# Optimization experiments

Hardware: AMD Instinct MI355X
Metric: run time of the kernel (lower is better)

The kernel has to match this reference:

```python
import jax, jax.numpy as jnp
import numpy as np

EMBED_DIM = 1024
NUM_HEADS = 16
HEAD_DIM = EMBED_DIM // NUM_HEADS
B, S = 2, 2048


def _xavier(k, shape):
    # xavier_uniform for square [out,in] weight
    limit = float(np.sqrt(6.0 / (shape[0] + shape[1])))
    return jax.random.uniform(k, shape, jnp.float32, -limit, limit)


def setup_inputs() -> dict:
    key = jax.random.key(0)
    ks = jax.random.split(key, 7)
    return {
        "query": jax.random.normal(ks[0], (B, S, EMBED_DIM), jnp.float32),
        "key": jax.random.normal(ks[1], (B, S, EMBED_DIM), jnp.float32),
        "value": jax.random.normal(ks[2], (B, S, EMBED_DIM), jnp.float32),
        "Wq": _xavier(ks[3], (EMBED_DIM, EMBED_DIM)),
        "Wk": _xavier(ks[4], (EMBED_DIM, EMBED_DIM)),
        "Wv": _xavier(ks[5], (EMBED_DIM, EMBED_DIM)),
        "Wo": _xavier(ks[6], (EMBED_DIM, EMBED_DIM)),
    }


def _orthogonalize(Wq, Wk):
    # Both projections computed from the ORIGINAL weights, then both replaced
    # (matches torch: weight1_proj/weight2_proj computed before copy_).
    Wq_o = Wq - Wq @ (Wk.T @ Wk)
    Wk_o = Wk - Wk @ (Wq.T @ Wq)
    return Wq_o, Wk_o


def reference(query, key, value, Wq, Wk, Wv, Wo):
    Wq_o, Wk_o = _orthogonalize(Wq, Wk)
    # F.linear(x, W) = x @ W.T
    q = query @ Wq_o.T
    k = key @ Wk_o.T
    v = value @ Wv.T
    # [B, S, E] -> [B, H, S, Dh]
    def split_heads(x):
        return x.reshape(B, -1, NUM_HEADS, HEAD_DIM).transpose(0, 2, 1, 3)
    q, k, v = split_heads(q), split_heads(k), split_heads(v)
    scale = 1.0 / (HEAD_DIM ** 0.5)
    scores = jnp.einsum("bhqd,bhkd->bhqk", q, k) * scale
    attn = jax.nn.softmax(scores, axis=-1)
    out = jnp.einsum("bhqk,bhkd->bhqd", attn, v)
    out = out.transpose(0, 2, 1, 3).reshape(B, -1, EMBED_DIM)
    return out @ Wo.T
```

## Files before the change

kernel.cpp:

```cpp
#include <hip/hip_runtime.h>
#include <math.h>

constexpr int EMBED  = 1024;
constexpr int NHEADS = 16;
constexpr int HDIM   = 64;
constexpr int BATCH  = 2;
constexpr int SEQ    = 2048;
constexpr int MROWS  = BATCH * SEQ;

typedef unsigned short u16b;
typedef __attribute__((ext_vector_type(8))) short bfrag;
typedef __attribute__((ext_vector_type(4))) float ffrag;
typedef __attribute__((ext_vector_type(16))) float f16frag;
typedef __attribute__((ext_vector_type(4))) int i32x4;

#define SCALE_Q 0.18033688f

__device__ __forceinline__ u16b f2b(float f) {
    union { float f; unsigned u; } v; v.f = f;
    unsigned r = v.u + 0x7fffu + ((v.u >> 16) & 1u);
    return (u16b)(r >> 16);
}

__device__ __forceinline__ unsigned cvtpk_bf16(float a, float b) {
    unsigned r;
    asm("v_cvt_pk_bf16_f32 %0, %1, %2" : "=v"(r) : "v"(a), "v"(b));
    return r;
}

__device__ __forceinline__ void plane_swap(unsigned a, unsigned b, int& lo, int& hi) {
    auto r = __builtin_amdgcn_permlane32_swap((int)a, (int)b, false, false);
    lo = (int)r[0];
    hi = (int)r[1];
}

__device__ __forceinline__ void gload_lds16(const u16b* g, u16b* l) {
    __builtin_amdgcn_global_load_lds(
        (const __attribute__((address_space(1))) void*)g,
        (__attribute__((address_space(3))) void*)l,
        16, 0, 0);
}

template<int N>
__device__ __forceinline__ void wait_vmcnt() {
    if constexpr (N == 0)      asm volatile("s_waitcnt vmcnt(0)" ::: "memory");
    else if constexpr (N == 3) asm volatile("s_waitcnt vmcnt(3)" ::: "memory");
    else if constexpr (N == 4) asm volatile("s_waitcnt vmcnt(4)" ::: "memory");
    else static_assert(N == 0 || N == 3 || N == 4, "unsupported vmcnt");
}

struct GemmPtrs {
    const u16b* A[3];
    const u16b* B[3];
    const float* D[3];
    u16b* Cb[3];
    float* Cf[3];
    float scale[3];
    int vt[3];
    int hs[3];
};

__global__ void prep_all(const float* __restrict__ q, const float* __restrict__ k,
                         const float* __restrict__ v,
                         const float* __restrict__ Wq, const float* __restrict__ Wk,
                         const float* __restrict__ Wv, const float* __restrict__ Wo,
                         u16b* __restrict__ oq, u16b* __restrict__ ok, u16b* __restrict__ ov,
                         u16b* __restrict__ wq, u16b* __restrict__ wk,
                         u16b* __restrict__ wv, u16b* __restrict__ wo,
                         u16b* __restrict__ wqt, u16b* __restrict__ wkt) {
    const int z = blockIdx.z;
    const int tid = threadIdx.x;
    if (z < 3) {
        const float* src = (z == 0) ? q : (z == 1) ? k : v;
        u16b* dst = (z == 0) ? oq : (z == 1) ? ok : ov;
        const int i = blockIdx.x * 256 + tid;
        float4 val = ((const float4*)src)[i];
        ushort4 o;
        o.x = f2b(val.x); o.y = f2b(val.y); o.z = f2b(val.z); o.w = f2b(val.w);
        ((ushort4*)dst)[i] = o;
        return;
    }
    if (blockIdx.x >= 1024) return;
    const int w = z - 3;
    const float* src = (w == 0) ? Wq : (w == 1) ? Wk : (w == 2) ? Wv : Wo;
    u16b* dst  = (w == 0) ? wq : (w == 1) ? wk : (w == 2) ? wv : wo;
    u16b* dstT = (w == 0) ? wqt : (w == 1) ? wkt : nullptr;
    __shared__ float t[32][33];
    const int bx = (blockIdx.x & 31) * 32, by = (blockIdx.x >> 5) * 32;
    const int x = tid & 31, y = tid >> 5;
#pragma unroll
    for (int r = 0; r < 4; ++r) {
        const int row = by + y + 8 * r;
        const float val = src[(size_t)row * EMBED + bx + x];
        dst[(size_t)row * EMBED + bx + x] = f2b(val);
        if (w < 2) t[y + 8 * r][x] = val;
    }
    if (w >= 2) return;
    __syncthreads();
#pragma unroll
    for (int r = 0; r < 4; ++r)
        dstT[(size_t)(bx + y + 8 * r) * EMBED + by + x] = f2b(t[x][y + 8 * r]);
}

template<int MODE, int BM>
__global__ __launch_bounds__(256) void gemm_big(GemmPtrs p, int M, int N, int K) {
    const int z = blockIdx.z;
    const u16b* __restrict__ A = p.A[z];
    const u16b* __restrict__ B = p.B[z];
    const float* __restrict__ D = p.D[z];
    u16b* __restrict__ Cb = p.Cb[z];
    float* __restrict__ Cf = p.Cf[z];
    const float scale = p.scale[z];
    const int vt = p.vt[z], hs = p.hs[z];

    constexpr int BK = 32;
    constexpr int IT = BM / 32;
    constexpr int IA = BM / 64;
    constexpr int LPW = IA + 2;
    __shared__ __align__(16) u16b As[2][BM * BK];
    __shared__ __align__(16) u16b Bs[2][128 * BK];

    const int tid = threadIdx.x;
    const int wave = tid >> 6, lane = tid & 63;
    const int quad = lane >> 4, l16 = lane & 15;
    const int wrow = wave >> 1, wcol = wave & 1;
    const int m0 = blockIdx.y * BM, n0 = blockIdx.x * 128;

    ffrag acc[IT][4];
#pragma unroll
    for (int i = 0; i < IT; ++i)
#pragma unroll
        for (int j = 0; j < 4; ++j) acc[i][j] = ffrag{0.f, 0.f, 0.f, 0.f};

    const int srow = lane >> 2, schunk = lane & 3;

    auto STAGE = [&](int buf, int kt) {
#pragma unroll
        for (int q = 0; q < IA; ++q) {
            int row = wave * (BM / 4) + q * 16;
            gload_lds16(A + (size_t)(m0 + row + srow) * K + kt + schunk * 8,
                        &As[buf][row * BK]);
        }
#pragma unroll
        for (int q = 0; q < 2; ++q) {
            int row = wave * 32 + q * 16;
            gload_lds16(B + (size_t)(n0 + row + srow) * K + kt + schunk * 8,
                        &Bs[buf][row * BK]);
        }
    };

    STAGE(0, 0);
    STAGE(1, BK);
    wait_vmcnt<LPW>();
    __builtin_amdgcn_s_barrier();
    __builtin_amdgcn_sched_barrier(0);

    int cur = 0;
    for (int kt = 0; kt < K; kt += BK, cur ^= 1) {
        bfrag af[IT], bfv[4];
#pragma unroll
        for (int i = 0; i < IT; ++i)
            af[i] = *(const bfrag*)&As[cur][(wrow * (BM / 2) + i * 16 + l16) * BK + quad * 8];
#pragma unroll
        for (int j = 0; j < 4; ++j)
            bfv[j] = *(const bfrag*)&Bs[cur][(wcol * 64 + j * 16 + l16) * BK + quad * 8];
        asm volatile("s_waitcnt lgkmcnt(0)" ::: "memory");
        __builtin_amdgcn_sched_barrier(0);
        __builtin_amdgcn_s_barrier();
        __builtin_amdgcn_sched_barrier(0);

        const bool stage = (kt + 2 * BK < K);
        if (stage) STAGE(cur, kt + 2 * BK);

#pragma unroll
        for (int i = 0; i < IT; ++i)
#pragma unroll
            for (int j = 0; j < 4; ++j)
                acc[i][j] = __builtin_amdgcn_mfma_f32_16x16x32_bf16(af[i], bfv[j], acc[i][j], 0, 0, 0);

        if (stage) wait_vmcnt<LPW>();
        else       wait_vmcnt<0>();
        __builtin_amdgcn_s_barrier();
        __builtin_amdgcn_sched_barrier(0);
    }

    if (MODE == 0 && vt) {
#pragma unroll
        for (int i = 0; i < IT; ++i)
#pragma unroll
            for (int j = 0; j < 4; ++j) {
                const int col = n0 + wcol * 64 + j * 16 + l16;
                const int h = col >> 6, d = col & 63;
                const int row0 = m0 + wrow * (BM / 2) + i * 16 + quad * 4;
                const int b = row0 >> 11, s = row0 & 2047;
                ushort4 o;
                o.x = f2b(acc[i][j][0]); o.y = f2b(acc[i][j][1]);
                o.z = f2b(acc[i][j][2]); o.w = f2b(acc[i][j][3]);
                *(ushort4*)&Cb[((size_t)(b * NHEADS + h) * HDIM + d) * SEQ + s] = o;
            }
        return;
    }
    if (MODE == 0 && hs) {
#pragma unroll
        for (int i = 0; i < IT; ++i)
#pragma unroll
            for (int j = 0; j < 4; ++j) {
                const int col = n0 + wcol * 64 + j * 16 + l16;
                const int h = col >> 6, d = col & 63;
                const int row0 = m0 + wrow * (BM / 2) + i * 16 + quad * 4;
                const int b = row0 >> 11, s0 = row0 & 2047;
#pragma unroll
                for (int r = 0; r < 4; ++r)
                    Cb[((size_t)(b * NHEADS + h) * SEQ + s0 + r) * HDIM + d] =
                        f2b(acc[i][j][r] * scale);
            }
        return;
    }

#pragma unroll
    for (int i = 0; i < IT; ++i)
#pragma unroll
        for (int j = 0; j < 4; ++j) {
            const int col = n0 + wcol * 64 + j * 16 + l16;
#pragma unroll
            for (int r = 0; r < 4; ++r) {
                const int row = m0 + wrow * (BM / 2) + i * 16 + quad * 4 + r;
                const size_t idx = (size_t)row * N + col;
                const float v = acc[i][j][r];
                if (MODE == 0) Cb[idx] = f2b(v * scale);
                else if (MODE == 1) Cb[idx] = f2b(D[idx] - v);
                else Cf[idx] = v;
            }
        }
}

__global__ __launch_bounds__(256) void flash_attn6(
    const u16b* __restrict__ Qp, const u16b* __restrict__ Kp,
    const u16b* __restrict__ Vt, float* __restrict__ Opart,
    float* __restrict__ Lpart)
{
    const int tid = threadIdx.x;
    const int wave = tid >> 6, lane = tid & 63;
    const int l32 = lane & 31, hi = lane >> 5;
    const int qt = blockIdx.x, h = blockIdx.y;
    const int b = blockIdx.z >> 1, sp = blockIdx.z & 1;
    const int qb = qt * 128 + wave * 32;
    const int kt0 = sp * (SEQ / 2), kt1 = kt0 + SEQ / 2;

    __shared__ __align__(16) u16b Ks[2][64 * 64];
    __shared__ __align__(16) u16b Vs[2][64 * 64];

    const size_t hsbase = (size_t)(b * NHEADS + h) * SEQ;
    const size_t vtbase = (size_t)(b * NHEADS + h) * HDIM * SEQ;
    const size_t obase  = ((size_t)sp * MROWS + (size_t)b * SEQ) * EMBED + h * HDIM;

    bfrag bq[4];
#pragma unroll
    for (int ks = 0; ks < 4; ++ks)
        bq[ks] = *(const bfrag*)&Qp[(hsbase + qb + l32) * HDIM + ks * 16 + hi * 8];

    f16frag ov0, ov1;
#pragma unroll
    for (int r = 0; r < 16; ++r) { ov0[r] = 0.f; ov1[r] = 0.f; }
    float l_run = 0.f;

    const int r0 = tid >> 3, c0 = tid & 7;
    const int sw0 = (r0 * 8 + (c0 ^ (r0 & 7))) * 8;
    const int sw1 = ((r0 + 32) * 8 + (c0 ^ (r0 & 7))) * 8;
    const u16b* kgb = Kp + hsbase * HDIM;
    const u16b* vgb = Vt + vtbase;

    {
        const u16b* kg = kgb + (size_t)kt0 * HDIM;
        bfrag k0 = *(const bfrag*)(kg + tid * 8);
        bfrag k1 = *(const bfrag*)(kg + (tid + 256) * 8);
        bfrag v0 = *(const bfrag*)(vgb + (size_t)r0 * SEQ + kt0 + c0 * 8);
        bfrag v1 = *(const bfrag*)(vgb + (size_t)(r0 + 32) * SEQ + kt0 + c0 * 8);
        *(bfrag*)&Ks[0][sw0] = k0;  *(bfrag*)&Ks[0][sw1] = k1;
        *(bfrag*)&Vs[0][sw0] = v0;  *(bfrag*)&Vs[0][sw1] = v1;
    }
    __syncthreads();

    int p = 0;
    for (int kt = kt0; kt < kt1; kt += 64, p ^= 1) {
        const bool more = (kt + 64) < kt1;
        bfrag kn0, kn1, vn0, vn1;
        if (more) {
            const u16b* kg = kgb + (size_t)(kt + 64) * HDIM;
            kn0 = *(const bfrag*)(kg + tid * 8);
            kn1 = *(const bfrag*)(kg + (tid + 256) * 8);
            vn0 = *(const bfrag*)(vgb + (size_t)r0 * SEQ + kt + 64 + c0 * 8);
            vn1 = *(const bfrag*)(vgb + (size_t)(r0 + 32) * SEQ + kt + 64 + c0 * 8);
        }

        f16frag St0, St1;
#pragma unroll
        for (int r = 0; r < 16; ++r) { St0[r] = 0.f; St1[r] = 0.f; }
#pragma unroll
        for (int ks = 0; ks < 4; ++ks) {
            const int ch = ks * 2 + hi;
            bfrag k0 = *(const bfrag*)&Ks[p][(l32 * 8 + (ch ^ (l32 & 7))) * 8];
            bfrag k1 = *(const bfrag*)&Ks[p][((32 + l32) * 8 + (ch ^ (l32 & 7))) * 8];
            St0 = __builtin_amdgcn_mfma_f32_32x32x16_bf16(k0, bq[ks], St0, 0, 0, 0);
            St1 = __builtin_amdgcn_mfma_f32_32x32x16_bf16(k1, bq[ks], St1, 0, 0, 0);
        }

        float rs = 0.f;
#pragma unroll
        for (int r = 0; r < 16; ++r) {
            const float a = __builtin_amdgcn_exp2f(St0[r]);
            const float c = __builtin_amdgcn_exp2f(St1[r]);
            St0[r] = a; St1[r] = c;
            rs += a + c;
        }
        rs += __shfl_xor(rs, 32);
        l_run += rs;

        unsigned d0[8], d1[8];
#pragma unroll
        for (int rr = 0; rr < 8; ++rr) {
            d0[rr] = cvtpk_bf16(St0[2 * rr], St0[2 * rr + 1]);
            d1[rr] = cvtpk_bf16(St1[2 * rr], St1[2 * rr + 1]);
        }
        bfrag bp[4];
        {
            int a0, a1, b0, b1, c0w, c1, e0, e1;
            plane_swap(d0[0], d0[2], a0, a1);
            plane_swap(d0[1], d0[3], b0, b1);
            i32x4 w = { a0, b0, a1, b1 };
            bp[0] = __builtin_bit_cast(bfrag, w);
            plane_swap(d0[4], d0[6], c0w, c1);
            plane_swap(d0[5], d0[7], e0, e1);
            i32x4 w2 = { c0w, e0, c1, e1 };
            bp[1] = __builtin_bit_cast(bfrag, w2);
        }
        {
            int a0, a1, b0, b1, c0w, c1, e0, e1;
            plane_swap(d1[0], d1[2], a0, a1);
            plane_swap(d1[1], d1[3], b0, b1);
            i32x4 w = { a0, b0, a1, b1 };
            bp[2] = __builtin_bit_cast(bfrag, w);
            plane_swap(d1[4], d1[6], c0w, c1);
            plane_swap(d1[5], d1[7], e0, e1);
            i32x4 w2 = { c0w, e0, c1, e1 };
            bp[3] = __builtin_bit_cast(bfrag, w2);
        }

#pragma unroll
        for (int ks = 0; ks < 4; ++ks) {
            const int ch = ks * 2 + hi;
            bfrag v0 = *(const bfrag*)&Vs[p][(l32 * 8 + (ch ^ (l32 & 7))) * 8];
            bfrag v1 = *(const bfrag*)&Vs[p][((32 + l32) * 8 + (ch ^ (l32 & 7))) * 8];
            ov0 = __builtin_amdgcn_mfma_f32_32x32x16_bf16(v0, bp[ks], ov0, 0, 0, 0);
            ov1 = __builtin_amdgcn_mfma_f32_32x32x16_bf16(v1, bp[ks], ov1, 0, 0, 0);
        }

        if (more) {
            *(bfrag*)&Ks[p ^ 1][sw0] = kn0;  *(bfrag*)&Ks[p ^ 1][sw1] = kn1;
            *(bfrag*)&Vs[p ^ 1][sw0] = vn0;  *(bfrag*)&Vs[p ^ 1][sw1] = vn1;
            __syncthreads();
        }
    }

    const size_t orow = obase + (size_t)(qb + l32) * EMBED;
#pragma unroll
    for (int rr = 0; rr < 4; ++rr) {
        float4 o0, o1;
        o0.x = ov0[4 * rr + 0]; o0.y = ov0[4 * rr + 1];
        o0.z = ov0[4 * rr + 2]; o0.w = ov0[4 * rr + 3];
        o1.x = ov1[4 * rr + 0]; o1.y = ov1[4 * rr + 1];
        o1.z = ov1[4 * rr + 2]; o1.w = ov1[4 * rr + 3];
        *(float4*)&Opart[orow + rr * 8 + hi * 4] = o0;
        *(float4*)&Opart[orow + 32 + rr * 8 + hi * 4] = o1;
    }
    if (hi == 0)
        Lpart[((size_t)sp * BATCH * NHEADS + b * NHEADS + h) * SEQ + qb + l32] = l_run;
}

__global__ void combine_o(const float* __restrict__ O0, const float* __restrict__ O1,
                          const float* __restrict__ L0, const float* __restrict__ L1,
                          u16b* __restrict__ ao) {
    const int i = blockIdx.x * 256 + threadIdx.x;
    const int e0 = i << 2;
    const int row = e0 >> 10, col = e0 & 1023;
    const int lidx = ((row >> 11) * NHEADS + (col >> 6)) * SEQ + (row & 2047);
    float4 a = ((const float4*)O0)[i];
    float4 c = ((const float4*)O1)[i];
    const float inv = 1.f / (L0[lidx] + L1[lidx]);
    ushort4 o;
    o.x = f2b((a.x + c.x) * inv); o.y = f2b((a.y + c.y) * inv);
    o.z = f2b((a.z + c.z) * inv); o.w = f2b((a.w + c.w) * inv);
    ((ushort4*)ao)[i] = o;
}

extern "C" void kernel_launch(void* const* d_in, const int* in_sizes, int n_in,
                              void* d_out, int out_size, void* d_ws, size_t ws_size,
                              hipStream_t stream) {
    const float* query = (const float*)d_in[0];
    const float* key_  = (const float*)d_in[1];
    const float* value = (const float*)d_in[2];
    const float* Wq    = (const float*)d_in[3];
    const float* Wk    = (const float*)d_in[4];
    const float* Wv    = (const float*)d_in[5];
    const float* Wo    = (const float*)d_in[6];
    float* out = (float*)d_out;

    char* ws = (char*)d_ws;
    const size_t MB = 1024 * 1024;
    u16b* xq  = (u16b*)(ws + 0 * MB);
    u16b* xk  = (u16b*)(ws + 8 * MB);
    u16b* xv  = (u16b*)(ws + 16 * MB);
    u16b* wq  = (u16b*)(ws + 24 * MB);
    u16b* wk  = (u16b*)(ws + 26 * MB);
    u16b* wv  = (u16b*)(ws + 28 * MB);
    u16b* gq  = (u16b*)(ws + 32 * MB);
    u16b* gk  = (u16b*)(ws + 34 * MB);
    u16b* wqo = (u16b*)(ws + 36 * MB);
    u16b* wko = (u16b*)(ws + 38 * MB);
    u16b* wo  = (u16b*)(ws + 40 * MB);
    u16b* qp  = (u16b*)(ws + 44 * MB);
    u16b* kp  = (u16b*)(ws + 52 * MB);
    u16b* Vt  = (u16b*)(ws + 60 * MB);
    u16b* wqt = (u16b*)(ws + 60 * MB);
    u16b* wkt = (u16b*)(ws + 62 * MB);
    float* Op  = (float*)(ws + 0 * MB);
    float* Lp  = (float*)(ws + 32 * MB);
    u16b*  ao  = (u16b*)(ws + 44 * MB);

    prep_all<<<dim3(MROWS * EMBED / 1024, 1, 7), dim3(256), 0, stream>>>(
        query, key_, value, Wq, Wk, Wv, Wo,
        xq, xk, xv, wq, wk, wv, wo, wqt, wkt);

    {
        GemmPtrs p{};
        p.A[0] = wqt; p.B[0] = wqt; p.Cb[0] = gq; p.scale[0] = 1.f;
        p.A[1] = wkt; p.B[1] = wkt; p.Cb[1] = gk; p.scale[1] = 1.f;
        gemm_big<0, 64><<<dim3(EMBED / 128, EMBED / 64, 2), dim3(256), 0, stream>>>(
            p, EMBED, EMBED, EMBED);
    }
    {
        GemmPtrs p{};
        p.A[0] = wq; p.B[0] = gk; p.D[0] = Wq; p.Cb[0] = wqo;
        p.A[1] = wk; p.B[1] = gq; p.D[1] = Wk; p.Cb[1] = wko;
        gemm_big<1, 64><<<dim3(EMBED / 128, EMBED / 64, 2), dim3(256), 0, stream>>>(
            p, EMBED, EMBED, EMBED);
    }
    {
        GemmPtrs p{};
        p.A[0] = xq; p.B[0] = wqo; p.Cb[0] = qp; p.scale[0] = SCALE_Q; p.hs[0] = 1;
        p.A[1] = xk; p.B[1] = wko; p.Cb[1] = kp; p.scale[1] = 1.f;     p.hs[1] = 1;
        p.A[2] = xv; p.B[2] = wv;  p.Cb[2] = Vt; p.scale[2] = 1.f;     p.vt[2] = 1;
        gemm_big<0, 128><<<dim3(EMBED / 128, MROWS / 128, 3), dim3(256), 0, stream>>>(
            p, MROWS, EMBED, EMBED);
    }
    flash_attn6<<<dim3(SEQ / 128, NHEADS, BATCH * 2), dim3(256), 0, stream>>>(
        qp, kp, Vt, Op, Lp);
    combine_o<<<dim3(MROWS * EMBED / 1024), dim3(256), 0, stream>>>(
        Op, Op + (size_t)MROWS * EMBED, Lp, Lp + (size_t)BATCH * NHEADS * SEQ, ao);
    {
        GemmPtrs p{};
        p.A[0] = ao; p.B[0] = wo; p.Cf[0] = out; p.scale[0] = 1.f;
        gemm_big<2, 64><<<dim3(EMBED / 128, MROWS / 64, 1), dim3(256), 0, stream>>>(
            p, MROWS, EMBED, EMBED);
    }
}
```

Baseline: 276.9 us.

## Load attention K/V fragments directly from global memory and add GEMM BN template

The flash attention kernel no longer stages K and V tiles through double-buffered shared memory with barriers. Each wave now loads its K and V MFMA fragments straight from global memory in 32-key steps and prefetches the next K fragments into registers. This removes LDS traffic and __syncthreads, but every wave now fetches K/V redundantly from global/L2 and gets less work per step. Separately, the GEMM gains a BN template parameter so the small weight-weight GEMMs use 64x64 tiles, giving more blocks.

```diff
diff --git a/kernel.cpp b/kernel.cpp
--- a/kernel.cpp
+++ b/kernel.cpp
@@ -44,9 +44,10 @@
 template<int N>
 __device__ __forceinline__ void wait_vmcnt() {
     if constexpr (N == 0)      asm volatile("s_waitcnt vmcnt(0)" ::: "memory");
+    else if constexpr (N == 2) asm volatile("s_waitcnt vmcnt(2)" ::: "memory");
     else if constexpr (N == 3) asm volatile("s_waitcnt vmcnt(3)" ::: "memory");
     else if constexpr (N == 4) asm volatile("s_waitcnt vmcnt(4)" ::: "memory");
-    else static_assert(N == 0 || N == 3 || N == 4, "unsupported vmcnt");
+    else static_assert(N == 0 || N == 2 || N == 3 || N == 4, "unsupported vmcnt");
 }
 
 struct GemmPtrs {
@@ -102,7 +103,7 @@
         dstT[(size_t)(bx + y + 8 * r) * EMBED + by + x] = f2b(t[x][y + 8 * r]);
 }
 
-template<int MODE, int BM>
+template<int MODE, int BM, int BN>
 __global__ __launch_bounds__(256) void gemm_big(GemmPtrs p, int M, int N, int K) {
     const int z = blockIdx.z;
     const u16b* __restrict__ A = p.A[z];
@@ -115,22 +116,24 @@
 
     constexpr int BK = 32;
     constexpr int IT = BM / 32;
+    constexpr int JT = BN / 32;
     constexpr int IA = BM / 64;
-    constexpr int LPW = IA + 2;
+    constexpr int IB = BN / 64;
+    constexpr int LPW = IA + IB;
     __shared__ __align__(16) u16b As[2][BM * BK];
-    __shared__ __align__(16) u16b Bs[2][128 * BK];
+    __shared__ __align__(16) u16b Bs[2][BN * BK];
 
     const int tid = threadIdx.x;
     const int wave = tid >> 6, lane = tid & 63;
     const int quad = lane >> 4, l16 = lane & 15;
     const int wrow = wave >> 1, wcol = wave & 1;
-    const int m0 = blockIdx.y * BM, n0 = blockIdx.x * 128;
-
-    ffrag acc[IT][4];
+    const int m0 = blockIdx.y * BM, n0 = blockIdx.x * BN;
+
+    ffrag acc[IT][JT];
 #pragma unroll
     for (int i = 0; i < IT; ++i)
 #pragma unroll
-        for (int j = 0; j < 4; ++j) acc[i][j] = ffrag{0.f, 0.f, 0.f, 0.f};
+        for (int j = 0; j < JT; ++j) acc[i][j] = ffrag{0.f, 0.f, 0.f, 0.f};
 
     const int srow = lane >> 2, schunk = lane & 3;
 
@@ -142,8 +145,8 @@
                         &As[buf][row * BK]);
         }
 #pragma unroll
-        for (int q = 0; q < 2; ++q) {
-            int row = wave * 32 + q * 16;
+        for (int q = 0; q < IB; ++q) {
+            int row = wave * (BN / 4) + q * 16;
             gload_lds16(B + (size_t)(n0 + row + srow) * K + kt + schunk * 8,
                         &Bs[buf][row * BK]);
         }
@@ -157,13 +160,13 @@
 
     int cur = 0;
     for (int kt = 0; kt < K; kt += BK, cur ^= 1) {
-        bfrag af[IT], bfv[4];
+        bfrag af[IT], bfv[JT];
 #pragma unroll
         for (int i = 0; i < IT; ++i)
             af[i] = *(const bfrag*)&As[cur][(wrow * (BM / 2) + i * 16 + l16) * BK + quad * 8];
 #pragma unroll
-        for (int j = 0; j < 4; ++j)
-            bfv[j] = *(const bfrag*)&Bs[cur][(wcol * 64 + j * 16 + l16) * BK + quad * 8];
+        for (int j = 0; j < JT; ++j)
+            bfv[j] = *(const bfrag*)&Bs[cur][(wcol * (BN / 2) + j * 16 + l16) * BK + quad * 8];
         asm volatile("s_waitcnt lgkmcnt(0)" ::: "memory");
         __builtin_amdgcn_sched_barrier(0);
         __builtin_amdgcn_s_barrier();
@@ -175,7 +178,7 @@
 #pragma unroll
         for (int i = 0; i < IT; ++i)
 #pragma unroll
-            for (int j = 0; j < 4; ++j)
+            for (int j = 0; j < JT; ++j)
                 acc[i][j] = __builtin_amdgcn_mfma_f32_16x16x32_bf16(af[i], bfv[j], acc[i][j], 0, 0, 0);
 
         if (stage) wait_vmcnt<LPW>();
@@ -188,8 +191,8 @@
 #pragma unroll
         for (int i = 0; i < IT; ++i)
 #pragma unroll
-            for (int j = 0; j < 4; ++j) {
-                const int col = n0 + wcol * 64 + j * 16 + l16;
+            for (int j = 0; j < JT; ++j) {
+                const int col = n0 + wcol * (BN / 2) + j * 16 + l16;
                 const int h = col >> 6, d = col & 63;
                 const int row0 = m0 + wrow * (BM / 2) + i * 16 + quad * 4;
                 const int b = row0 >> 11, s = row0 & 2047;
@@ -204,8 +207,8 @@
 #pragma unroll
         for (int i = 0; i < IT; ++i)
 #pragma unroll
-            for (int j = 0; j < 4; ++j) {
-                const int col = n0 + wcol * 64 + j * 16 + l16;
+            for (int j = 0; j < JT; ++j) {
+                const int col = n0 + wcol * (BN / 2) + j * 16 + l16;
                 const int h = col >> 6, d = col & 63;
                 const int row0 = m0 + wrow * (BM / 2) + i * 16 + quad * 4;
                 const int b = row0 >> 11, s0 = row0 & 2047;
@@ -220,8 +223,8 @@
 #pragma unroll
     for (int i = 0; i < IT; ++i)
 #pragma unroll
-        for (int j = 0; j < 4; ++j) {
-            const int col = n0 + wcol * 64 + j * 16 + l16;
+        for (int j = 0; j < JT; ++j) {
+            const int col = n0 + wcol * (BN / 2) + j * 16 + l16;
 #pragma unroll
             for (int r = 0; r < 4; ++r) {
                 const int row = m0 + wrow * (BM / 2) + i * 16 + quad * 4 + r;
@@ -234,7 +237,7 @@
         }
 }
 
-__global__ __launch_bounds__(256) void flash_attn6(
+__global__ __launch_bounds__(256) void flash_attn7(
     const u16b* __restrict__ Qp, const u16b* __restrict__ Kp,
     const u16b* __restrict__ Vt, float* __restrict__ Opart,
     float* __restrict__ Lpart)
@@ -247,9 +250,6 @@
     const int qb = qt * 128 + wave * 32;
     const int kt0 = sp * (SEQ / 2), kt1 = kt0 + SEQ / 2;
 
-    __shared__ __align__(16) u16b Ks[2][64 * 64];
-    __shared__ __align__(16) u16b Vs[2][64 * 64];
-
     const size_t hsbase = (size_t)(b * NHEADS + h) * SEQ;
     const size_t vtbase = (size_t)(b * NHEADS + h) * HDIM * SEQ;
     const size_t obase  = ((size_t)sp * MROWS + (size_t)b * SEQ) * EMBED + h * HDIM;
@@ -264,101 +264,71 @@
     for (int r = 0; r < 16; ++r) { ov0[r] = 0.f; ov1[r] = 0.f; }
     float l_run = 0.f;
 
-    const int r0 = tid >> 3, c0 = tid & 7;
-    const int sw0 = (r0 * 8 + (c0 ^ (r0 & 7))) * 8;
-    const int sw1 = ((r0 + 32) * 8 + (c0 ^ (r0 & 7))) * 8;
     const u16b* kgb = Kp + hsbase * HDIM;
     const u16b* vgb = Vt + vtbase;
 
-    {
-        const u16b* kg = kgb + (size_t)kt0 * HDIM;
-        bfrag k0 = *(const bfrag*)(kg + tid * 8);
-        bfrag k1 = *(const bfrag*)(kg + (tid + 256) * 8);
-        bfrag v0 = *(const bfrag*)(vgb + (size_t)r0 * SEQ + kt0 + c0 * 8);
-        bfrag v1 = *(const bfrag*)(vgb + (size_t)(r0 + 32) * SEQ + kt0 + c0 * 8);
-        *(bfrag*)&Ks[0][sw0] = k0;  *(bfrag*)&Ks[0][sw1] = k1;
-        *(bfrag*)&Vs[0][sw0] = v0;  *(bfrag*)&Vs[0][sw1] = v1;
-    }
-    __syncthreads();
-
-    int p = 0;
-    for (int kt = kt0; kt < kt1; kt += 64, p ^= 1) {
-        const bool more = (kt + 64) < kt1;
-        bfrag kn0, kn1, vn0, vn1;
+    bfrag kf[4];
+#pragma unroll
+    for (int ks = 0; ks < 4; ++ks)
+        kf[ks] = *(const bfrag*)&kgb[(size_t)(kt0 + l32) * HDIM + ks * 16 + hi * 8];
+
+    for (int kt = kt0; kt < kt1; kt += 32) {
+        f16frag St;
+#pragma unroll
+        for (int r = 0; r < 16; ++r) St[r] = 0.f;
+#pragma unroll
+        for (int ks = 0; ks < 4; ++ks)
+            St = __builtin_amdgcn_mfma_f32_32x32x16_bf16(kf[ks], bq[ks], St, 0, 0, 0);
+
+        bfrag vf0[2], vf1[2], kn[4];
+        const bool more = (kt + 32) < kt1;
+#pragma unroll
+        for (int s = 0; s < 2; ++s) {
+            vf0[s] = *(const bfrag*)&vgb[(size_t)l32 * SEQ + kt + s * 16 + hi * 8];
+            vf1[s] = *(const bfrag*)&vgb[(size_t)(32 + l32) * SEQ + kt + s * 16 + hi * 8];
+        }
         if (more) {
-            const u16b* kg = kgb + (size_t)(kt + 64) * HDIM;
-            kn0 = *(const bfrag*)(kg + tid * 8);
-            kn1 = *(const bfrag*)(kg + (tid + 256) * 8);
-            vn0 = *(const bfrag*)(vgb + (size_t)r0 * SEQ + kt + 64 + c0 * 8);
-            vn1 = *(const bfrag*)(vgb + (size_t)(r0 + 32) * SEQ + kt + 64 + c0 * 8);
-        }
-
-        f16frag St0, St1;
-#pragma unroll
-        for (int r = 0; r < 16; ++r) { St0[r] = 0.f; St1[r] = 0.f; }
-#pragma unroll
-        for (int ks = 0; ks < 4; ++ks) {
-            const int ch = ks * 2 + hi;
-            bfrag k0 = *(const bfrag*)&Ks[p][(l32 * 8 + (ch ^ (l32 & 7))) * 8];
-            bfrag k1 = *(const bfrag*)&Ks[p][((32 + l32) * 8 + (ch ^ (l32 & 7))) * 8];
-            St0 = __builtin_amdgcn_mfma_f32_32x32x16_bf16(k0, bq[ks], St0, 0, 0, 0);
-            St1 = __builtin_amdgcn_mfma_f32_32x32x16_bf16(k1, bq[ks], St1, 0, 0, 0);
+#pragma unroll
+            for (int ks = 0; ks < 4; ++ks)
+                kn[ks] = *(const bfrag*)&kgb[(size_t)(kt + 32 + l32) * HDIM + ks * 16 + hi * 8];
         }
 
         float rs = 0.f;
 #pragma unroll
         for (int r = 0; r < 16; ++r) {
-            const float a = __builtin_amdgcn_exp2f(St0[r]);
-            const float c = __builtin_amdgcn_exp2f(St1[r]);
-            St0[r] = a; St1[r] = c;
-            rs += a + c;
+            const float e = __builtin_amdgcn_exp2f(St[r]);
+            St[r] = e;
+            rs += e;
         }
         rs += __shfl_xor(rs, 32);
         l_run += rs;
 
-        unsigned d0[8], d1[8];
-#pragma unroll
-        for (int rr = 0; rr < 8; ++rr) {
-            d0[rr] = cvtpk_bf16(St0[2 * rr], St0[2 * rr + 1]);
-            d1[rr] = cvtpk_bf16(St1[2 * rr], St1[2 * rr + 1]);
-        }
-        bfrag bp[4];
+        unsigned d[8];
+#pragma unroll
+        for (int rr = 0; rr < 8; ++rr)
+            d[rr] = cvtpk_bf16(St[2 * rr], St[2 * rr + 1]);
+        bfrag bp[2];
         {
             int a0, a1, b0, b1, c0w, c1, e0, e1;
-            plane_swap(d0[0], d0[2], a0, a1);
-            plane_swap(d0[1], d0[3], b0, b1);
+            plane_swap(d[0], d[2], a0, a1);
+            plane_swap(d[1], d[3], b0, b1);
             i32x4 w = { a0, b0, a1, b1 };
             bp[0] = __builtin_bit_cast(bfrag, w);
-            plane_swap(d0[4], d0[6], c0w, c1);
-            plane_swap(d0[5], d0[7], e0, e1);
+            plane_swap(d[4], d[6], c0w, c1);
+            plane_swap(d[5], d[7], e0, e1);
             i32x4 w2 = { c0w, e0, c1, e1 };
             bp[1] = __builtin_bit_cast(bfrag, w2);
         }
-        {
-            int a0, a1, b0, b1, c0w, c1, e0, e1;
-            plane_swap(d1[0], d1[2], a0, a1);
-            plane_swap(d1[1], d1[3], b0, b1);
-            i32x4 w = { a0, b0, a1, b1 };
-            bp[2] = __builtin_bit_cast(bfrag, w);
-            plane_swap(d1[4], d1[6], c0w, c1);
-            plane_swap(d1[5], d1[7], e0, e1);
-            i32x4 w2 = { c0w, e0, c1, e1 };
-            bp[3] = __builtin_bit_cast(bfrag, w2);
-        }
-
-#pragma unroll
-        for (int ks = 0; ks < 4; ++ks) {
-            const int ch = ks * 2 + hi;
-            bfrag v0 = *(const bfrag*)&Vs[p][(l32 * 8 + (ch ^ (l32 & 7))) * 8];
-            bfrag v1 = *(const bfrag*)&Vs[p][((32 + l32) * 8 + (ch ^ (l32 & 7))) * 8];
-            ov0 = __builtin_amdgcn_mfma_f32_32x32x16_bf16(v0, bp[ks], ov0, 0, 0, 0);
-            ov1 = __builtin_amdgcn_mfma_f32_32x32x16_bf16(v1, bp[ks], ov1, 0, 0, 0);
+
+#pragma unroll
+        for (int s = 0; s < 2; ++s) {
+            ov0 = __builtin_amdgcn_mfma_f32_32x32x16_bf16(vf0[s], bp[s], ov0, 0, 0, 0);
+            ov1 = __builtin_amdgcn_mfma_f32_32x32x16_bf16(vf1[s], bp[s], ov1, 0, 0, 0);
         }
 
         if (more) {
-            *(bfrag*)&Ks[p ^ 1][sw0] = kn0;  *(bfrag*)&Ks[p ^ 1][sw1] = kn1;
-            *(bfrag*)&Vs[p ^ 1][sw0] = vn0;  *(bfrag*)&Vs[p ^ 1][sw1] = vn1;
-            __syncthreads();
+#pragma unroll
+            for (int ks = 0; ks < 4; ++ks) kf[ks] = kn[ks];
         }
     }
 
@@ -435,14 +405,14 @@
         GemmPtrs p{};
         p.A[0] = wqt; p.B[0] = wqt; p.Cb[0] = gq; p.scale[0] = 1.f;
         p.A[1] = wkt; p.B[1] = wkt; p.Cb[1] = gk; p.scale[1] = 1.f;
-        gemm_big<0, 64><<<dim3(EMBED / 128, EMBED / 64, 2), dim3(256), 0, stream>>>(
+        gemm_big<0, 64, 64><<<dim3(EMBED / 64, EMBED / 64, 2), dim3(256), 0, stream>>>(
             p, EMBED, EMBED, EMBED);
     }
     {
         GemmPtrs p{};
         p.A[0] = wq; p.B[0] = gk; p.D[0] = Wq; p.Cb[0] = wqo;
         p.A[1] = wk; p.B[1] = gq; p.D[1] = Wk; p.Cb[1] = wko;
-        gemm_big<1, 64><<<dim3(EMBED / 128, EMBED / 64, 2), dim3(256), 0, stream>>>(
+        gemm_big<1, 64, 64><<<dim3(EMBED / 64, EMBED / 64, 2), dim3(256), 0, stream>>>(
             p, EMBED, EMBED, EMBED);
     }
     {
@@ -450,17 +420,17 @@
         p.A[0] = xq; p.B[0] = wqo; p.Cb[0] = qp; p.scale[0] = SCALE_Q; p.hs[0] = 1;
         p.A[1] = xk; p.B[1] = wko; p.Cb[1] = kp; p.scale[1] = 1.f;     p.hs[1] = 1;
         p.A[2] = xv; p.B[2] = wv;  p.Cb[2] = Vt; p.scale[2] = 1.f;     p.vt[2] = 1;
-        gemm_big<0, 128><<<dim3(EMBED / 128, MROWS / 128, 3), dim3(256), 0, stream>>>(
+        gemm_big<0, 128, 128><<<dim3(EMBED / 128, MROWS / 128, 3), dim3(256), 0, stream>>>(
             p, MROWS, EMBED, EMBED);
     }
-    flash_attn6<<<dim3(SEQ / 128, NHEADS, BATCH * 2), dim3(256), 0, stream>>>(
+    flash_attn7<<<dim3(SEQ / 128, NHEADS, BATCH * 2), dim3(256), 0, stream>>>(
         qp, kp, Vt, Op, Lp);
     combine_o<<<dim3(MROWS * EMBED / 1024), dim3(256), 0, stream>>>(
         Op, Op + (size_t)MROWS * EMBED, Lp, Lp + (size_t)BATCH * NHEADS * SEQ, ao);
     {
         GemmPtrs p{};
         p.A[0] = ao; p.B[0] = wo; p.Cf[0] = out; p.scale[0] = 1.f;
-        gemm_big<2, 64><<<dim3(EMBED / 128, MROWS / 64, 1), dim3(256), 0, stream>>>(
+        gemm_big<2, 64, 128><<<dim3(EMBED / 128, MROWS / 64, 1), dim3(256), 0, stream>>>(
             p, MROWS, EMBED, EMBED);
     }
 }
```

Measured after the change: 337.8 us. +22.0%, slower.
